# Kernel tuning notes

Hardware: AMD Instinct MI355X
Metric: run time of the kernel (lower is better)

The kernel has to match this reference:

```python
import jax, jax.numpy as jnp
import numpy as np

NUM_OUT_POINTS = 1024  # init kwarg num_out_points


def setup_inputs() -> dict:
    key = jax.random.key(0)
    x = jax.random.normal(key, (128, 3, 32768), dtype=jnp.float32)
    return {"x": x}


def _fps_indices(pts, k):
    """Furthest point sampling. pts: [B, N, 3] -> idx [B, k] int32.
    Matches the standard CUDA kernel: start at point 0, iteratively pick the
    point with max min-distance to the selected set."""
    B, N, _ = pts.shape
    idx0 = jnp.zeros((B,), jnp.int32)
    mindist0 = jnp.full((B, N), 1e10, pts.dtype)

    def step(carry, _):
        mindist, last = carry
        # coordinates of the most recently selected point: [B, 1, 3]
        p_last = jnp.take_along_axis(pts, last[:, None, None], axis=1)
        d = jnp.sum((pts - p_last) ** 2, axis=-1)          # [B, N]
        mindist = jnp.minimum(mindist, d)
        nxt = jnp.argmax(mindist, axis=-1).astype(jnp.int32)
        return (mindist, nxt), nxt

    (_, _), rest = jax.lax.scan(step, (mindist0, idx0), None, length=k - 1)
    # rest: [k-1, B]; prepend the initial index 0
    return jnp.concatenate([idx0[None, :], rest], axis=0).T  # [B, k]


def reference(x):
    # x: [B, 3, N]; permute=False so y = x
    pts = jnp.transpose(x, (0, 2, 1))                      # [B, N, 3]
    idx = _fps_indices(pts, NUM_OUT_POINTS)                # [B, k]
    y = jnp.take_along_axis(pts, idx[..., None], axis=1)   # [B, k, 3]
    return jnp.transpose(y, (0, 2, 1))                     # [B, 3, k]
```

## Files before the change

kernel.cpp:

```cpp
#include <hip/hip_runtime.h>

#define BATCH    128
#define NPTS     32768
#define KOUT     1024
#define NTHREADS 1024
#define PPT      (NPTS / NTHREADS)

extern __shared__ float s_md[];

__global__ __launch_bounds__(NTHREADS)
__attribute__((amdgpu_waves_per_eu(4, 4)))
void fps_kernel(const float* __restrict__ x, float* __restrict__ out) {
    __shared__ float s_redv[16];
    __shared__ int   s_redi[16];
    __shared__ float s_pt[3];

    const int b   = blockIdx.x;
    const int tid = threadIdx.x;
    const float* __restrict__ xb = x + (size_t)b * 3 * NPTS;
    float* __restrict__ ob = out + (size_t)b * 3 * KOUT;

    float xs[PPT], ys[PPT], zs[PPT];
#pragma unroll
    for (int i = 0; i < PPT; ++i) {
        const int n = tid + i * NTHREADS;
        xs[i] = xb[n];
        ys[i] = xb[NPTS + n];
        zs[i] = xb[2 * NPTS + n];
        s_md[n] = 1e10f;
    }

    float px = xb[0], py = xb[NPTS], pz = xb[2 * NPTS];
    if (tid == 0) {
        ob[0] = px; ob[KOUT] = py; ob[2 * KOUT] = pz;
    }
    __syncthreads();

    const int lane = tid & 63;
    const int wave = tid >> 6;

    for (int j = 1; j < KOUT; ++j) {
        float best = -1.0f;
        int   bi   = 0x7fffffff;

#pragma unroll
        for (int i = 0; i < PPT; ++i) {
            const int n = tid + i * NTHREADS;
            const float dx = __fsub_rn(xs[i], px);
            const float dy = __fsub_rn(ys[i], py);
            const float dz = __fsub_rn(zs[i], pz);
            const float d  = __fmaf_rn(dz, dz,
                              __fmaf_rn(dy, dy,
                                __fmul_rn(dx, dx)));
            const float m  = fminf(s_md[n], d);
            s_md[n] = m;
            if (m > best) { best = m; bi = n; }
        }

#pragma unroll
        for (int s = 1; s < 64; s <<= 1) {
            const float ov = __shfl_xor(best, s, 64);
            const int   oi = __shfl_xor(bi,   s, 64);
            if (ov > best || (ov == best && oi < bi)) { best = ov; bi = oi; }
        }
        if (lane == 0) { s_redv[wave] = best; s_redi[wave] = bi; }
        __syncthreads();

        if (wave == 0) {
            float v  = (lane < 16) ? s_redv[lane] : -1.0f;
            int   vi = (lane < 16) ? s_redi[lane] : 0x7fffffff;
#pragma unroll
            for (int s = 1; s < 16; s <<= 1) {
                const float ov = __shfl_xor(v,  s, 64);
                const int   oi = __shfl_xor(vi, s, 64);
                if (ov > v || (ov == v && oi < vi)) { v = ov; vi = oi; }
            }
            if (lane == 0) {
                const float sx = xb[vi];
                const float sy = xb[NPTS + vi];
                const float sz = xb[2 * NPTS + vi];
                s_pt[0] = sx; s_pt[1] = sy; s_pt[2] = sz;
                ob[j] = sx; ob[KOUT + j] = sy; ob[2 * KOUT + j] = sz;
            }
        }
        __syncthreads();
        px = s_pt[0]; py = s_pt[1]; pz = s_pt[2];
    }
}

extern "C" void kernel_launch(void* const* d_in, const int* in_sizes, int n_in,
                              void* d_out, int out_size, void* d_ws, size_t ws_size,
                              hipStream_t stream) {
    const float* x = (const float*)d_in[0];
    float* out = (float*)d_out;

    const size_t dyn_lds = (size_t)NPTS * sizeof(float);
    hipFuncSetAttribute((const void*)fps_kernel,
                        hipFuncAttributeMaxDynamicSharedMemorySize,
                        (int)dyn_lds);
    fps_kernel<<<BATCH, NTHREADS, dyn_lds, stream>>>(x, out);
}
```

Before: 3.604 ms.

## Keep coordinates in AGPRs and min-distances in VGPRs instead of LDS

Point coordinates are parked in accumulation registers through inline asm and read back on every iteration. The per-point min-distance array moves from LDS into VGPRs, which removes an LDS read and write per point per step. This drops the dynamic shared memory allocation and the waves_per_eu attribute. It costs extra accvgpr read instructions and raises register pressure, with 96 AGPR values and 32 VGPR values per thread, so spilling is a risk.

Result: slower. 4.852 ms (+34.6%).

```diff
diff --git a/kernel.cpp b/kernel.cpp
--- a/kernel.cpp
+++ b/kernel.cpp
@@ -6,10 +6,7 @@
 #define NTHREADS 1024
 #define PPT      (NPTS / NTHREADS)
 
-extern __shared__ float s_md[];
-
 __global__ __launch_bounds__(NTHREADS)
-__attribute__((amdgpu_waves_per_eu(4, 4)))
 void fps_kernel(const float* __restrict__ x, float* __restrict__ out) {
     __shared__ float s_redv[16];
     __shared__ int   s_redi[16];
@@ -20,21 +17,26 @@
     const float* __restrict__ xb = x + (size_t)b * 3 * NPTS;
     float* __restrict__ ob = out + (size_t)b * 3 * KOUT;
 
-    float xs[PPT], ys[PPT], zs[PPT];
+    float xa[PPT], ya[PPT], za[PPT];
 #pragma unroll
     for (int i = 0; i < PPT; ++i) {
         const int n = tid + i * NTHREADS;
-        xs[i] = xb[n];
-        ys[i] = xb[NPTS + n];
-        zs[i] = xb[2 * NPTS + n];
-        s_md[n] = 1e10f;
+        float vx = xb[n];
+        float vy = xb[NPTS + n];
+        float vz = xb[2 * NPTS + n];
+        asm volatile("v_accvgpr_write_b32 %0, %1" : "=a"(xa[i]) : "v"(vx));
+        asm volatile("v_accvgpr_write_b32 %0, %1" : "=a"(ya[i]) : "v"(vy));
+        asm volatile("v_accvgpr_write_b32 %0, %1" : "=a"(za[i]) : "v"(vz));
     }
+
+    float md[PPT];
+#pragma unroll
+    for (int i = 0; i < PPT; ++i) md[i] = 1e10f;
 
     float px = xb[0], py = xb[NPTS], pz = xb[2 * NPTS];
     if (tid == 0) {
         ob[0] = px; ob[KOUT] = py; ob[2 * KOUT] = pz;
     }
-    __syncthreads();
 
     const int lane = tid & 63;
     const int wave = tid >> 6;
@@ -45,16 +47,19 @@
 
 #pragma unroll
         for (int i = 0; i < PPT; ++i) {
-            const int n = tid + i * NTHREADS;
-            const float dx = __fsub_rn(xs[i], px);
-            const float dy = __fsub_rn(ys[i], py);
-            const float dz = __fsub_rn(zs[i], pz);
+            float cx, cy, cz;
+            asm volatile("v_accvgpr_read_b32 %0, %1" : "=v"(cx) : "a"(xa[i]));
+            asm volatile("v_accvgpr_read_b32 %0, %1" : "=v"(cy) : "a"(ya[i]));
+            asm volatile("v_accvgpr_read_b32 %0, %1" : "=v"(cz) : "a"(za[i]));
+            const float dx = __fsub_rn(cx, px);
+            const float dy = __fsub_rn(cy, py);
+            const float dz = __fsub_rn(cz, pz);
             const float d  = __fmaf_rn(dz, dz,
                               __fmaf_rn(dy, dy,
                                 __fmul_rn(dx, dx)));
-            const float m  = fminf(s_md[n], d);
-            s_md[n] = m;
-            if (m > best) { best = m; bi = n; }
+            const float m  = fminf(md[i], d);
+            md[i] = m;
+            if (m > best) { best = m; bi = tid + i * NTHREADS; }
         }
 
 #pragma unroll
@@ -93,10 +98,5 @@
                               hipStream_t stream) {
     const float* x = (const float*)d_in[0];
     float* out = (float*)d_out;
-
-    const size_t dyn_lds = (size_t)NPTS * sizeof(float);
-    hipFuncSetAttribute((const void*)fps_kernel,
-                        hipFuncAttributeMaxDynamicSharedMemorySize,
-                        (int)dyn_lds);
-    fps_kernel<<<BATCH, NTHREADS, dyn_lds, stream>>>(x, out);
+    fps_kernel<<<BATCH, NTHREADS, 0, stream>>>(x, out);
 }
```

## Use contiguous per-thread points with float4 swizzled LDS min-distance and skipped stores

Applied to the files above, without the earlier changes.

Each thread now owns a contiguous run of points and keeps its min-distance array in LDS as XOR-swizzled float4 slots, so every access is a 128-bit LDS load or store instead of a scalar one. A store is skipped when no lane in the wave lowered any distance in the slot. The waves-per-EU attribute and the dynamic shared memory setup are dropped in favour of static LDS. This aims to cut LDS instruction count and traffic in the inner loop, at the cost of uncoalesced strided global loads during setup and some extra compare and ballot work.

New measurement: 6.179 ms. +71.5%, slower.

```diff
diff --git a/kernel.cpp b/kernel.cpp
--- a/kernel.cpp
+++ b/kernel.cpp
@@ -5,30 +5,34 @@
 #define KOUT     1024
 #define NTHREADS 1024
 #define PPT      (NPTS / NTHREADS)
-
-extern __shared__ float s_md[];
+#define NBLK     (PPT / 4)
 
 __global__ __launch_bounds__(NTHREADS)
-__attribute__((amdgpu_waves_per_eu(4, 4)))
 void fps_kernel(const float* __restrict__ x, float* __restrict__ out) {
-    __shared__ float s_redv[16];
-    __shared__ int   s_redi[16];
-    __shared__ float s_pt[3];
+    __shared__ float4 s_md4[NPTS / 4];
+    __shared__ float  s_redv[16];
+    __shared__ int    s_redi[16];
+    __shared__ float  s_pt[3];
 
     const int b   = blockIdx.x;
     const int tid = threadIdx.x;
     const float* __restrict__ xb = x + (size_t)b * 3 * NPTS;
     float* __restrict__ ob = out + (size_t)b * 3 * KOUT;
 
+    const int tid7  = tid & 7;
+    const int sbase = tid * NBLK;
+
     float xs[PPT], ys[PPT], zs[PPT];
 #pragma unroll
     for (int i = 0; i < PPT; ++i) {
-        const int n = tid + i * NTHREADS;
+        const int n = tid * PPT + i;
         xs[i] = xb[n];
         ys[i] = xb[NPTS + n];
         zs[i] = xb[2 * NPTS + n];
-        s_md[n] = 1e10f;
     }
+#pragma unroll
+    for (int k = 0; k < NBLK; ++k)
+        s_md4[sbase + k] = make_float4(1e10f, 1e10f, 1e10f, 1e10f);
 
     float px = xb[0], py = xb[NPTS], pz = xb[2 * NPTS];
     if (tid == 0) {
@@ -44,17 +48,28 @@
         int   bi   = 0x7fffffff;
 
 #pragma unroll
-        for (int i = 0; i < PPT; ++i) {
-            const int n = tid + i * NTHREADS;
-            const float dx = __fsub_rn(xs[i], px);
-            const float dy = __fsub_rn(ys[i], py);
-            const float dz = __fsub_rn(zs[i], pz);
-            const float d  = __fmaf_rn(dz, dz,
-                              __fmaf_rn(dy, dy,
-                                __fmul_rn(dx, dx)));
-            const float m  = fminf(s_md[n], d);
-            s_md[n] = m;
-            if (m > best) { best = m; bi = n; }
+        for (int k = 0; k < NBLK; ++k) {
+            const int slot = sbase + (k ^ tid7);
+            const float4 mo = s_md4[slot];
+            float m[4];
+#pragma unroll
+            for (int q = 0; q < 4; ++q) {
+                const int i = 4 * k + q;
+                const float dx = __fsub_rn(xs[i], px);
+                const float dy = __fsub_rn(ys[i], py);
+                const float dz = __fsub_rn(zs[i], pz);
+                const float d  = __fmaf_rn(dz, dz,
+                                  __fmaf_rn(dy, dy,
+                                    __fmul_rn(dx, dx)));
+                const float o  = (q == 0) ? mo.x : (q == 1) ? mo.y
+                               : (q == 2) ? mo.z : mo.w;
+                m[q] = fminf(o, d);
+                if (m[q] > best) { best = m[q]; bi = tid * PPT + i; }
+            }
+            const bool chg = (m[0] < mo.x) || (m[1] < mo.y) ||
+                             (m[2] < mo.z) || (m[3] < mo.w);
+            if (__any(chg))
+                s_md4[slot] = make_float4(m[0], m[1], m[2], m[3]);
         }
 
 #pragma unroll
@@ -93,10 +108,5 @@
                               hipStream_t stream) {
     const float* x = (const float*)d_in[0];
     float* out = (float*)d_out;
-
-    const size_t dyn_lds = (size_t)NPTS * sizeof(float);
-    hipFuncSetAttribute((const void*)fps_kernel,
-                        hipFuncAttributeMaxDynamicSharedMemorySize,
-                        (int)dyn_lds);
-    fps_kernel<<<BATCH, NTHREADS, dyn_lds, stream>>>(x, out);
+    fps_kernel<<<BATCH, NTHREADS, 0, stream>>>(x, out);
 }
```
